# Kernel optimization log

Measured on AMD Instinct MI355X. Metric: run time of the kernel, lower is better.

The kernel has to match this reference:

```python
import jax, jax.numpy as jnp
from jax import lax
import numpy as np

BLOCK = 256
EPS = 1e-6


def rms_norm(x, w):
    var = jnp.mean(jnp.square(x), axis=-1, keepdims=True)
    return x * lax.rsqrt(var + EPS) * w


def lightning_attn(q, k, v, slope):
    # q,k,v: [b,h,n,d]; slope: [h] positive decay rates
    b, h, n, d = q.shape
    nb = n // BLOCK
    ar = jnp.arange(1, BLOCK + 1, dtype=q.dtype)          # [BLOCK]
    s = slope[:, None, None]                               # [h,1,1]
    q_decay = jnp.exp(-s * ar[:, None])                    # [h,BLOCK,1]
    k_decay = jnp.exp(-s * (BLOCK - ar)[:, None])          # [h,BLOCK,1]
    idx = ar[:, None] - ar[None, :]                        # [BLOCK,BLOCK]
    diag_decay = jnp.exp(jnp.where(idx >= 0, -s * idx, -jnp.inf))  # [h,B,B]
    block_decay = jnp.exp(-slope * BLOCK)[None, :, None, None]     # [1,h,1,1]

    def to_blocks(x):
        return jnp.moveaxis(x.reshape(b, h, nb, BLOCK, d), 2, 0)   # [nb,b,h,B,d]

    qb, kb, vb = to_blocks(q), to_blocks(k), to_blocks(v)

    def step(kv, blk):
        qi, ki, vi = blk                                   # [b,h,B,d]
        inter = jnp.einsum('bhmd,bhde->bhme', qi * q_decay, kv)
        qk = jnp.einsum('bhmd,bhkd->bhmk', qi, ki) * diag_decay
        intra = jnp.einsum('bhmk,bhke->bhme', qk, vi)
        kv_new = block_decay * kv + jnp.einsum('bhmd,bhme->bhde', ki * k_decay, vi)
        return kv_new, inter + intra

    kv0 = jnp.zeros((b, h, d, d), q.dtype)
    kv, out = lax.scan(step, kv0, (qb, kb, vb))            # out: [nb,b,h,B,d]
    out = jnp.moveaxis(out, 0, 2).reshape(b, h, n, d)
    return out, kv


def setup_inputs() -> dict:
    key = jax.random.key(0)
    ks = jax.random.split(key, 6)
    b, n, hidden, h, dh = 2, 4096, 2048, 16, 128
    return {
        'hidden_states': jax.random.normal(ks[0], (b, n, hidden), jnp.float32),
        'slope_rate': jax.random.uniform(ks[1], (h,), jnp.float32, 1e-3, 0.2),
        'w_qkv': jax.random.normal(ks[2], (3 * h * dh, hidden), jnp.float32) * 0.02,
        'w_gate': jax.random.normal(ks[3], (h * dh, hidden), jnp.float32) * 0.02,
        'w_out': jax.random.normal(ks[4], (hidden, h * dh), jnp.float32) * 0.02,
        'norm_w': jnp.ones((h * dh,), jnp.float32),
    }


def reference(hidden_states, slope_rate, w_qkv, w_gate, w_out, norm_w):
    b, n, hidden = hidden_states.shape
    h = slope_rate.shape[0]
    dh = hidden // h
    qkv = jax.nn.silu(hidden_states @ w_qkv.T)             # [b,n,3*h*dh]
    qkv = qkv.reshape(b, n, 3, h, dh)
    q = jnp.transpose(qkv[:, :, 0], (0, 2, 1, 3))          # [b,h,n,dh]
    k = jnp.transpose(qkv[:, :, 1], (0, 2, 1, 3))
    v = jnp.transpose(qkv[:, :, 2], (0, 2, 1, 3))
    attn_out, _kv = lightning_attn(q, k, v, slope_rate)
    attn_out = jnp.transpose(attn_out, (0, 2, 1, 3)).reshape(b, n, h * dh)
    out = rms_norm(attn_out, norm_w)
    gate = jax.nn.sigmoid(hidden_states @ w_gate.T)
    out = (gate * out) @ w_out.T
    return out
```

## Files before the change

kernel.cpp:

```cpp
#include <hip/hip_runtime.h>


typedef unsigned short u16;
typedef __bf16 bf16x8 __attribute__((ext_vector_type(8)));
typedef float f32x4 __attribute__((ext_vector_type(4)));

#define SEQ 4096
#define HID 2048

__device__ __forceinline__ u16 f2bf(float f) {
    union { float f; unsigned u; } v; v.f = f;
    unsigned r = v.u + 0x7fffu + ((v.u >> 16) & 1u);
    return (u16)(r >> 16);
}
__device__ __forceinline__ float bf2f(u16 u) {
    union { unsigned u; float f; } v; v.u = ((unsigned)u) << 16; return v.f;
}

typedef __attribute__((address_space(1))) unsigned char gas_u8;
typedef __attribute__((address_space(3))) unsigned char las_u8;
__device__ __forceinline__ void gld16(const void* g, void* l) {
    __builtin_amdgcn_global_load_lds((gas_u8*)g, (las_u8*)l, 16, 0, 0);
}

__global__ __launch_bounds__(256) void castk3(const float* __restrict__ a, u16* __restrict__ ao,
                                              const float* __restrict__ b, u16* __restrict__ bo,
                                              const float* __restrict__ c, u16* __restrict__ co) {
    const int bid = blockIdx.x;
    const float* src; u16* dst; size_t i;
    if (bid < 16384)      { src = a; dst = ao; i = (size_t)bid * 256 + threadIdx.x; }
    else if (bid < 28672) { src = b; dst = bo; i = (size_t)(bid - 16384) * 256 + threadIdx.x; }
    else                  { src = c; dst = co; i = (size_t)(bid - 28672) * 256 + threadIdx.x; }
    const float4 f = *(const float4*)&src[i * 4];
    uint2 o;
    o.x = (unsigned)f2bf(f.x) | ((unsigned)f2bf(f.y) << 16);
    o.y = (unsigned)f2bf(f.z) | ((unsigned)f2bf(f.w) << 16);
    *(uint2*)&dst[i * 4] = o;
}

template <int MODE>
__global__ __launch_bounds__(512, 2) void gemm256(const u16* __restrict__ A,
                                                  const u16* __restrict__ Bm,
                                                  void* __restrict__ Cv,
                                                  void* __restrict__ aux,
                                                  void* __restrict__ aux2) {
    constexpr int NTN = (MODE == 0) ? 32 : 8;
    constexpr int NT  = 32;
    extern __shared__ u16 smem[];

    const int bid = blockIdx.x;
    const int xcd = bid & 7, l = bid >> 3;
    int tm, tn;
    if constexpr (MODE == 0) {
        tm = xcd * 4 + (l & 3);
        tn = ((l >> 2) & 7) | ((l >> 5) << 3);
    } else {
        const int wgid = xcd * 32 + l;
        tm = wgid / NTN; tn = wgid % NTN;
    }

    const int tid  = threadIdx.x;
    const int lane = tid & 63, wv = tid >> 6;
    const int quad = lane >> 4, cl = lane & 15;
    const int wm = (wv & 1) * 128, wn = (wv >> 1) * 64;

    const int srw  = tid >> 3;
    const int colo = ((tid & 7) ^ (srw & 7)) * 8;
    const u16* gA0 = A  + (size_t)(tm * 256 + srw) * HID + colo;
    const u16* gB0 = Bm + (size_t)(tn * 256 + srw) * HID + colo;

    const int x0 = ((quad       ^ (cl & 7)) * 8);
    const int x1 = (((4 + quad) ^ (cl & 7)) * 8);

    f32x4 acc[8][4];
    const f32x4 zero = {0.f, 0.f, 0.f, 0.f};
    #pragma unroll
    for (int a = 0; a < 8; a++)
        #pragma unroll
        for (int b = 0; b < 4; b++) acc[a][b] = zero;

    bf16x8 af[8], b0[4], b1[4];

    auto STG = [&](int kt, int mat, int hh) {
        const u16* g = (mat ? gB0 : gA0) + (size_t)(hh * 128) * HID + kt * 64;
        u16* lp = smem + (kt & 1) * 32768 + mat * 16384 + hh * 8192 + wv * 512;
        gld16(g, lp);
        gld16(g + (size_t)64 * HID, lp + 4096);
    };
    auto LDA = [&](int qm, int ab) {
        #pragma unroll
        for (int mi = 0; mi < 4; mi++) {
            const int rr = (wm + qm * 64 + mi * 16 + cl) * 64 + ab;
            af[mi * 2 + 0] = *(const bf16x8*)&smem[rr + x0];
            af[mi * 2 + 1] = *(const bf16x8*)&smem[rr + x1];
        }
    };
    auto LDB = [&](bf16x8* d, int qn, int bb2) {
        #pragma unroll
        for (int ni = 0; ni < 2; ni++) {
            const int rr = (wn + qn * 32 + ni * 16 + cl) * 64 + bb2;
            d[ni * 2 + 0] = *(const bf16x8*)&smem[rr + x0];
            d[ni * 2 + 1] = *(const bf16x8*)&smem[rr + x1];
        }
    };
    auto MM = [&](int qm, int qn, const bf16x8* bv) {
        #pragma unroll
        for (int mi = 0; mi < 4; mi++)
            #pragma unroll
            for (int ni = 0; ni < 2; ni++) {
                f32x4 c = acc[qm * 4 + mi][qn * 2 + ni];
                c = __builtin_amdgcn_mfma_f32_16x16x32_bf16(af[mi * 2 + 0], bv[ni * 2 + 0], c, 0, 0, 0);
                c = __builtin_amdgcn_mfma_f32_16x16x32_bf16(af[mi * 2 + 1], bv[ni * 2 + 1], c, 0, 0, 0);
                acc[qm * 4 + mi][qn * 2 + ni] = c;
            }
    };

    STG(0, 1, 0); STG(0, 1, 1); STG(0, 0, 0); STG(0, 0, 1);
    STG(1, 1, 0); STG(1, 1, 1); STG(1, 0, 0);
    asm volatile("s_waitcnt vmcnt(6)" ::: "memory");
    __builtin_amdgcn_s_barrier();
    LDA(0, 0); LDB(b0, 0, 16384);

    #pragma unroll 2
    for (int t = 0; t < NT; ++t) {
        const int ab  = (t & 1) * 32768;
        const int bb2 = ab + 16384;
        const int nab = ((t + 1) & 1) * 32768;
        if (t + 1 < NT) STG(t + 1, 0, 1);
        __builtin_amdgcn_s_barrier();
        asm volatile("s_waitcnt lgkmcnt(0)" ::: "memory");
        __builtin_amdgcn_s_setprio(1); MM(0, 0, b0); __builtin_amdgcn_s_setprio(0);
        LDB(b1, 1, bb2);
        __builtin_amdgcn_s_barrier();
        if (t + 2 < NT) STG(t + 2, 1, 0);
        __builtin_amdgcn_s_barrier();
        asm volatile("s_waitcnt lgkmcnt(0)" ::: "memory");
        __builtin_amdgcn_s_setprio(1); MM(0, 1, b1); __builtin_amdgcn_s_setprio(0);
        LDA(1, ab);
        __builtin_amdgcn_s_barrier();
        if (t + 2 < NT) STG(t + 2, 1, 1);
        __builtin_amdgcn_s_barrier();
        asm volatile("s_waitcnt lgkmcnt(0)" ::: "memory");
        __builtin_amdgcn_s_setprio(1); MM(1, 1, b1); __builtin_amdgcn_s_setprio(0);
        __builtin_amdgcn_s_barrier();
        if (t + 2 < NT) {
            STG(t + 2, 0, 0);
            asm volatile("s_waitcnt vmcnt(6)" ::: "memory");
        } else {
            asm volatile("s_waitcnt vmcnt(0)" ::: "memory");
        }
        __builtin_amdgcn_s_barrier();
        __builtin_amdgcn_s_setprio(1); MM(1, 0, b0); __builtin_amdgcn_s_setprio(0);
        if (t + 1 < NT) { LDA(0, nab); LDB(b0, 0, nab + 16384); }
        __builtin_amdgcn_s_barrier();
    }

    if constexpr (MODE == 0) {
        const int grp = tn * 2 + (wn >> 7);
        const int which = grp >> 4, hd = grp & 15;
        const int n64 = wn & 64;
        if (which == 2) {
            const size_t bz = (size_t)((tm >> 4) * 256 + hd * 16 + (tm & 15));
            u16* tdst = (u16*)aux + bz * 32768;
            #pragma unroll
            for (int a = 0; a < 8; a++) {
                const int mm = wm + (a >> 2) * 64 + (a & 3) * 16 + quad * 4;
                #pragma unroll
                for (int b = 0; b < 4; b++) {
                    const int d = n64 + (b >> 1) * 32 + (b & 1) * 16 + cl;
                    u16 p[4];
                    #pragma unroll
                    for (int r = 0; r < 4; r++) {
                        const float x = acc[a][b][r];
                        p[r] = f2bf(x / (1.f + __expf(-x)));
                    }
                    uint2 pk;
                    pk.x = (unsigned)p[0] | ((unsigned)p[1] << 16);
                    pk.y = (unsigned)p[2] | ((unsigned)p[3] << 16);
                    *(uint2*)&tdst[(size_t)d * 256 + mm] = pk;
                }
            }
            return;
        }
        u16* dst = (which == 0) ? (u16*)Cv
                 : (which == 1) ? (u16*)Cv + (size_t)16777216
                                : (u16*)aux2;
        #pragma unroll
        for (int a = 0; a < 8; a++)
            #pragma unroll
            for (int b = 0; b < 4; b++)
                #pragma unroll
                for (int r = 0; r < 4; r++) {
                    const int m = tm * 256 + wm + (a >> 2) * 64 + (a & 3) * 16 + quad * 4 + r;
                    const int col = hd * 128 + n64 + (b >> 1) * 32 + (b & 1) * 16 + cl;
                    const float x = acc[a][b][r];
                    const float v = (which == 3) ? 1.f / (1.f + __expf(-x))
                                                 : x / (1.f + __expf(-x));
                    dst[(size_t)m * HID + col] = f2bf(v);
                }
        return;
    } else {
        float* C = (float*)Cv;
        #pragma unroll
        for (int a = 0; a < 8; a++)
            #pragma unroll
            for (int b = 0; b < 4; b++)
                #pragma unroll
                for (int r = 0; r < 4; r++) {
                    const int m = tm * 256 + wm + (a >> 2) * 64 + (a & 3) * 16 + quad * 4 + r;
                    const int n = tn * 256 + wn + (b >> 1) * 32 + (b & 1) * 16 + cl;
                    C[(size_t)m * HID + n] = acc[a][b][r];
                }
    }
}

#define M_KVT   4

template <int MODE>
__global__ __launch_bounds__(256) void gemm_nt(const u16* __restrict__ A,
                                               const u16* __restrict__ Bm,
                                               void* __restrict__ Cv,
                                               const float* __restrict__ slope,
                                               int bz0,
                                               void* __restrict__ aux,
                                               void* __restrict__ aux2) {
    const int tid = threadIdx.x;
    const int bz  = blockIdx.z + bz0;

    __shared__ u16 smem[16384];

    const int lane = tid & 63, wv = tid >> 6;
    const int wm = (wv & 1) * 64, wn = (wv >> 1) * 64;
    const int quad = lane >> 4, cl = lane & 15;
    const int lr = lane >> 2;
    const int lc = (lane & 3) * 8;

    f32x4 acc[4][4];
    const f32x4 zero = {0.f, 0.f, 0.f, 0.f};
    #pragma unroll
    for (int mi = 0; mi < 4; mi++)
        #pragma unroll
        for (int ni = 0; ni < 4; ni++) acc[mi][ni] = zero;

    const u16* gA = A  + (size_t)bz * 32768 + (size_t)(wv * 32 + lr) * 256 + lc;
    const u16* gB = Bm + (size_t)bz * 32768 + (size_t)(wv * 32 + lr) * 256 + lc;

    auto stage = [&](int c, int buf) {
        u16* lA = smem + buf * 8192 + wv * 1024;
        u16* lB = lA + 4096;
        const int k0 = c * 32;
        gld16(gA + k0,                    lA);
        gld16(gA + k0 + (size_t)16 * 256, lA + 512);
        gld16(gB + k0,                    lB);
        gld16(gB + k0 + (size_t)16 * 256, lB + 512);
    };

    stage(0, 0);
    for (int c = 0; c < 8; ++c) {
        const int cb = c & 1;
        if (c + 1 < 8) {
            stage(c + 1, cb ^ 1);
            asm volatile("s_waitcnt vmcnt(4)" ::: "memory");
        } else {
            asm volatile("s_waitcnt vmcnt(0)" ::: "memory");
        }
        __builtin_amdgcn_s_barrier();
        const u16* As = smem + cb * 8192;
        const u16* Bs = As + 4096;
        const int ko = quad * 8;
        bf16x8 af[4], bfv[4];
        #pragma unroll
        for (int mi = 0; mi < 4; mi++) af[mi] = *(const bf16x8*)&As[(wm + mi * 16 + cl) * 32 + ko];
        #pragma unroll
        for (int ni = 0; ni < 4; ni++) bfv[ni] = *(const bf16x8*)&Bs[(wn + ni * 16 + cl) * 32 + ko];
        #pragma unroll
        for (int mi = 0; mi < 4; mi++)
            #pragma unroll
            for (int ni = 0; ni < 4; ni++)
                acc[mi][ni] = __builtin_amdgcn_mfma_f32_16x16x32_bf16(af[mi], bfv[ni], acc[mi][ni], 0, 0, 0);
        __builtin_amdgcn_s_barrier();
    }

    #pragma unroll
    for (int mi = 0; mi < 4; mi++)
        #pragma unroll
        for (int ni = 0; ni < 4; ni++)
            #pragma unroll
            for (int r = 0; r < 4; r++) {
                const int m = wm + mi * 16 + quad * 4 + r;
                const int n = wn + ni * 16 + cl;
                ((float*)Cv)[(size_t)bz * 16384 + m * 128 + n] = acc[mi][ni][r];
            }
}

__global__ __launch_bounds__(256) void fused_pv(const u16* __restrict__ qb,
                                                const u16* __restrict__ kb,
                                                const u16* __restrict__ ST,
                                                const u16* __restrict__ vT,
                                                u16* __restrict__ attn,
                                                const float* __restrict__ slope) {
    __shared__ u16 smem[36864];
    u16* q_lds = smem;
    u16* k_lds = smem + 16384;
    u16* P_lds = smem + 24576;
    u16* Bs    = smem + 28672;

    const int tm = blockIdx.x;
    const int bz = blockIdx.z;
    const int bb = bz >> 8, hh = (bz >> 4) & 15, jb = bz & 15;
    const float s_ = slope[hh];

    const int tid  = threadIdx.x;
    const int lane = tid & 63, wv = tid >> 6;
    const int quad = lane >> 4, cl = lane & 15;
    const int wm = (wv & 1) * 64, wn = (wv >> 1) * 64;
    const int lr = lane >> 2, lc = (lane & 3) * 8;
    const int pcb = (wv >> 1) * 16;

    const size_t rowbase = (size_t)(bb * SEQ + jb * 256);

    const u16* gq = qb + (rowbase + tm * 128 + wv * 32 + lr) * HID + hh * 128 + lc;
    u16* lq = q_lds + wv * 1024 + lr * 32 + lc;
    #pragma unroll
    for (int ks = 0; ks < 4; ks++) {
        gld16(gq + ks * 32,                 lq + ks * 4096);
        gld16(gq + ks * 32 + 16 * HID,      lq + ks * 4096 + 512);
    }

    f32x4 acc[4][4];
    const f32x4 zero = {0.f, 0.f, 0.f, 0.f};
    #pragma unroll
    for (int mi = 0; mi < 4; mi++)
        #pragma unroll
        for (int ni = 0; ni < 4; ni++) acc[mi][ni] = zero;

    const u16* gS = ST + (size_t)bz * 16384 + (size_t)(wv * 32 + lr) * 128 + lc;
    auto stage_st = [&](int ks, int buf) {
        u16* lB = Bs + buf * 4096 + wv * 1024 + lr * 32 + lc;
        gld16(gS + ks * 32,            lB);
        gld16(gS + ks * 32 + 16 * 128, lB + 512);
    };
    stage_st(0, 0);
    #pragma unroll
    for (int ks = 0; ks < 4; ks++) {
        const int sb = ks & 1;
        if (ks + 1 < 4) {
            stage_st(ks + 1, sb ^ 1);
            asm volatile("s_waitcnt vmcnt(2)" ::: "memory");
        } else {
            asm volatile("s_waitcnt vmcnt(0)" ::: "memory");
        }
        __builtin_amdgcn_s_barrier();
        bf16x8 af[4], bfv[4];
        #pragma unroll
        for (int mi = 0; mi < 4; mi++)
            af[mi] = *(const bf16x8*)&q_lds[ks * 4096 + (wm + mi * 16 + cl) * 32 + quad * 8];
        #pragma unroll
        for (int ni = 0; ni < 4; ni++)
            bfv[ni] = *(const bf16x8*)&Bs[sb * 4096 + (wn + ni * 16 + cl) * 32 + quad * 8];
        #pragma unroll
        for (int mi = 0; mi < 4; mi++)
            #pragma unroll
            for (int ni = 0; ni < 4; ni++)
                acc[mi][ni] = __builtin_amdgcn_mfma_f32_16x16x32_bf16(af[mi], bfv[ni], acc[mi][ni], 0, 0, 0);
        __builtin_amdgcn_s_barrier();
    }
    #pragma unroll
    for (int mi = 0; mi < 4; mi++)
        #pragma unroll
        for (int r = 0; r < 4; r++) {
            const int m = tm * 128 + wm + mi * 16 + quad * 4 + r;
            const float qd = __expf(-s_ * (float)(m + 1));
            #pragma unroll
            for (int ni = 0; ni < 4; ni++) acc[mi][ni][r] *= qd;
        }

    const int kmax = (tm == 0) ? 128 : 256;
    const int nc   = kmax >> 5;
    const u16* gV = vT + (size_t)bz * 32768 + (size_t)(wv * 32 + lr) * 256 + lc;
    const int krow = tid >> 4;
    const int kcol = (((tid & 15) ^ (krow & 7)) * 8);
    const int kvr = pcb + cl;

    auto stage_chunk = [&](int c, int buf) {
        u16* lk = k_lds + buf * 4096 + wv * 512 + lane * 8;
        u16* lv = Bs + buf * 4096 + wv * 1024 + lr * 32 + lc;
        const int kv0 = c * 32;
        gld16(kb + (rowbase + kv0 +      krow) * HID + hh * 128 + kcol, lk);
        gld16(kb + (rowbase + kv0 + 16 + krow) * HID + hh * 128 + kcol, lk + 2048);
        gld16(gV + kv0,            lv);
        gld16(gV + kv0 + 16 * 256, lv + 512);
    };

    stage_chunk(0, 0);
    for (int c = 0; c < nc; ++c) {
        const int cb = c & 1;
        if (c + 1 < nc) {
            stage_chunk(c + 1, cb ^ 1);
            asm volatile("s_waitcnt vmcnt(4)" ::: "memory");
        } else {
            asm volatile("s_waitcnt vmcnt(0)" ::: "memory");
        }
        __builtin_amdgcn_s_barrier();
        f32x4 acc2[4];
        #pragma unroll
        for (int mi = 0; mi < 4; mi++) acc2[mi] = zero;
        #pragma unroll
        for (int ds = 0; ds < 4; ds++) {
            bf16x8 bk = *(const bf16x8*)&k_lds[cb * 4096 + kvr * 128 + (((ds * 4 + quad) ^ (kvr & 7)) * 8)];
            #pragma unroll
            for (int mi = 0; mi < 4; mi++) {
                bf16x8 aq = *(const bf16x8*)&q_lds[ds * 4096 + (wm + mi * 16 + cl) * 32 + quad * 8];
                acc2[mi] = __builtin_amdgcn_mfma_f32_16x16x32_bf16(aq, bk, acc2[mi], 0, 0, 0);
            }
        }
        const int kv0 = c * 32;
        #pragma unroll
        for (int mi = 0; mi < 4; mi++)
            #pragma unroll
            for (int r = 0; r < 4; r++) {
                const int row = wm + mi * 16 + quad * 4 + r;
                const int mb  = tm * 128 + row;
                const int kv  = kv0 + pcb + cl;
                const int d   = mb - kv;
                const float x = acc2[mi][r];
                P_lds[row * 32 + pcb + cl] = f2bf(d >= 0 ? x * __expf(-s_ * (float)d) : 0.f);
            }
        asm volatile("s_waitcnt lgkmcnt(0)" ::: "memory");
        __builtin_amdgcn_s_barrier();
        bf16x8 afp[4], bfv[4];
        #pragma unroll
        for (int mi = 0; mi < 4; mi++)
            afp[mi] = *(const bf16x8*)&P_lds[(wm + mi * 16 + cl) * 32 + quad * 8];
        #pragma unroll
        for (int ni = 0; ni < 4; ni++)
            bfv[ni] = *(const bf16x8*)&Bs[cb * 4096 + (wn + ni * 16 + cl) * 32 + quad * 8];
        #pragma unroll
        for (int mi = 0; mi < 4; mi++)
            #pragma unroll
            for (int ni = 0; ni < 4; ni++)
                acc[mi][ni] = __builtin_amdgcn_mfma_f32_16x16x32_bf16(afp[mi], bfv[ni], acc[mi][ni], 0, 0, 0);
        __builtin_amdgcn_s_barrier();
    }

    #pragma unroll
    for (int mi = 0; mi < 4; mi++)
        #pragma unroll
        for (int ni = 0; ni < 4; ni++)
            #pragma unroll
            for (int r = 0; r < 4; r++) {
                const int m = tm * 128 + wm + mi * 16 + quad * 4 + r;
                const int n = wn + ni * 16 + cl;
                attn[(rowbase + m) * HID + hh * 128 + n] = f2bf(acc[mi][ni][r]);
            }
}

__global__ __launch_bounds__(256) void transpose_k(const u16* __restrict__ kb,
                                                   u16* __restrict__ kTs,
                                                   const float* __restrict__ slope) {
    __shared__ u16 t[128][137];
    const int bz = blockIdx.x;
    const int bb = bz >> 8, hh = (bz >> 4) & 15, jb = bz & 15;
    const int tid = threadIdx.x;
    const float s_ = slope[hh];
    const u16* src = kb + ((size_t)(bb * SEQ + jb * 256)) * HID + hh * 128;
    u16* dst = kTs + (size_t)bz * 32768;

    for (int half = 0; half < 2; half++) {
        #pragma unroll
        for (int i = 0; i < 8; i++) {
            const int flat = tid + 256 * i;
            const int row = flat >> 4, c8 = (flat & 15) * 8;
            *(uint4*)&t[row][c8] = *(const uint4*)&src[(size_t)(half * 128 + row) * HID + c8];
        }
        __syncthreads();
        #pragma unroll
        for (int i = 0; i < 8; i++) {
            const int flat = tid + 256 * i;
            const int d = flat >> 4, mc = (flat & 15) * 8;
            u16 p[8];
            #pragma unroll
            for (int j = 0; j < 8; j++) {
                const int m = half * 128 + mc + j;
                p[j] = f2bf(bf2f(t[mc + j][d]) * __expf(-s_ * (float)(255 - m)));
            }
            uint4 pk;
            pk.x = (unsigned)p[0] | ((unsigned)p[1] << 16);
            pk.y = (unsigned)p[2] | ((unsigned)p[3] << 16);
            pk.z = (unsigned)p[4] | ((unsigned)p[5] << 16);
            pk.w = (unsigned)p[6] | ((unsigned)p[7] << 16);
            *(uint4*)&dst[(size_t)d * 256 + half * 128 + mc] = pk;
        }
        __syncthreads();
    }
}

__global__ __launch_bounds__(256) void scan_kv(const float* __restrict__ KVT,
                                               u16* __restrict__ ST,
                                               const float* __restrict__ slope) {
    const int bh = blockIdx.x >> 4, ch = blockIdx.x & 15;
    const int off = ch * 1024 + threadIdx.x * 4;
    const float bd = __expf(-256.f * slope[bh & 15]);
    float4 st = {0.f, 0.f, 0.f, 0.f};
    for (int j = 0; j < 16; j++) {
        const size_t base = ((size_t)(bh * 16 + j)) * 16384 + off;
        uint2 o;
        o.x = (unsigned)f2bf(st.x) | ((unsigned)f2bf(st.y) << 16);
        o.y = (unsigned)f2bf(st.z) | ((unsigned)f2bf(st.w) << 16);
        *(uint2*)&ST[base] = o;
        const float4 kv = *(const float4*)&KVT[base];
        st.x = bd * st.x + kv.x;
        st.y = bd * st.y + kv.y;
        st.z = bd * st.z + kv.z;
        st.w = bd * st.w + kv.w;
    }
}

__global__ __launch_bounds__(256) void rmsnorm_gate(const u16* __restrict__ attn,
                                                    const u16* __restrict__ gate,
                                                    const float* __restrict__ nw,
                                                    u16* __restrict__ y,
                                                    const float* __restrict__ wout,
                                                    u16* __restrict__ wout_bf) {
    const int r = blockIdx.x, tid = threadIdx.x;

    {
        const size_t wi = (size_t)r * 512 + tid * 2;
        const float2 wf = *(const float2*)&wout[wi];
        *(unsigned*)&wout_bf[wi] = (unsigned)f2bf(wf.x) | ((unsigned)f2bf(wf.y) << 16);
    }

    const size_t base = (size_t)r * HID + tid * 8;
    const uint4 a = *(const uint4*)&attn[base];
    float x[8];
    x[0] = bf2f(a.x & 0xffff); x[1] = bf2f(a.x >> 16);
    x[2] = bf2f(a.y & 0xffff); x[3] = bf2f(a.y >> 16);
    x[4] = bf2f(a.z & 0xffff); x[5] = bf2f(a.z >> 16);
    x[6] = bf2f(a.w & 0xffff); x[7] = bf2f(a.w >> 16);
    float s = 0.f;
    #pragma unroll
    for (int i = 0; i < 8; i++) s += x[i] * x[i];
    #pragma unroll
    for (int off = 32; off > 0; off >>= 1) s += __shfl_down(s, off);
    __shared__ float red[4];
    if ((tid & 63) == 0) red[tid >> 6] = s;
    __syncthreads();
    const float tot = red[0] + red[1] + red[2] + red[3];
    const float sc = rsqrtf(tot * (1.f / 2048.f) + 1e-6f);
    const uint4 g = *(const uint4*)&gate[base];
    float gv[8];
    gv[0] = bf2f(g.x & 0xffff); gv[1] = bf2f(g.x >> 16);
    gv[2] = bf2f(g.y & 0xffff); gv[3] = bf2f(g.y >> 16);
    gv[4] = bf2f(g.z & 0xffff); gv[5] = bf2f(g.z >> 16);
    gv[6] = bf2f(g.w & 0xffff); gv[7] = bf2f(g.w >> 16);
    const float4 w0 = *(const float4*)&nw[tid * 8];
    const float4 w1 = *(const float4*)&nw[tid * 8 + 4];
    const float wv[8] = {w0.x, w0.y, w0.z, w0.w, w1.x, w1.y, w1.z, w1.w};
    u16 o[8];
    #pragma unroll
    for (int i = 0; i < 8; i++) o[i] = f2bf(gv[i] * x[i] * sc * wv[i]);
    uint4 ov;
    ov.x = (unsigned)o[0] | ((unsigned)o[1] << 16);
    ov.y = (unsigned)o[2] | ((unsigned)o[3] << 16);
    ov.z = (unsigned)o[4] | ((unsigned)o[5] << 16);
    ov.w = (unsigned)o[6] | ((unsigned)o[7] << 16);
    *(uint4*)&y[base] = ov;
}

extern "C" void kernel_launch(void* const* d_in, const int* in_sizes, int n_in,
                              void* d_out, int out_size, void* d_ws, size_t ws_size,
                              hipStream_t stream) {
    const float* hidden = (const float*)d_in[0];
    const float* slope  = (const float*)d_in[1];
    const float* w_qkv  = (const float*)d_in[2];
    const float* w_gate = (const float*)d_in[3];
    const float* w_out  = (const float*)d_in[4];
    const float* norm_w = (const float*)d_in[5];
    float* out = (float*)d_out;

    char* w = (char*)d_ws;
    u16* qb   = (u16*)(w);
    u16* kb   = (u16*)(w +  33554432);
    u16* kTs  = (u16*)(w +  67108864);
    u16* hid_bf = (u16*)(w + 100663296);
    u16* vT   = (u16*)(w + 134217728);
    u16* gate = (u16*)(w + 167772160);
    u16* wqkv_bf  = (u16*)(w + 201326592);
    u16* wgate_bf = (u16*)(w + 201326592 + 25165824);
    float* KVT  = (float*)hid_bf;
    u16*   ST   = kTs;
    u16*   wout_bf = kb;
    u16*   attn = wqkv_bf;
    u16*   y    = kTs;

    static bool s_attr = false;
    if (!s_attr) {
        (void)hipFuncSetAttribute((const void*)gemm256<0>,
                                  hipFuncAttributeMaxDynamicSharedMemorySize, 131072);
        (void)hipFuncSetAttribute((const void*)gemm256<1>,
                                  hipFuncAttributeMaxDynamicSharedMemorySize, 131072);
        s_attr = true;
    }

    castk3<<<32768, 256, 0, stream>>>(hidden, hid_bf, w_qkv, wqkv_bf, w_gate, wgate_bf);

    gemm256<0><<<dim3(1024), dim3(512), 131072, stream>>>(hid_bf, wqkv_bf, qb, vT, gate);
    transpose_k     <<<512,             256, 0, stream>>>(kb, kTs, slope);
    gemm_nt<M_KVT ><<<dim3(1, 1, 512),  256, 0, stream>>>(vT, kTs, KVT, slope, 0, nullptr, nullptr);
    scan_kv         <<<512,             256, 0, stream>>>(KVT, ST, slope);
    fused_pv        <<<dim3(2, 1, 512), 256, 0, stream>>>(qb, kb, ST, vT, attn, slope);
    rmsnorm_gate    <<<8192,            256, 0, stream>>>(attn, gate, norm_w, y, w_out, wout_bf);
    gemm256<1><<<dim3(256), dim3(512), 131072, stream>>>(y, wout_bf, (void*)out, nullptr, nullptr);
}
```

Before: 441.6 us.

## Fuse K transpose and decay scaling into the per-block KV GEMM

Removes the separate transpose_k kernel, which wrote a decayed, transposed copy of K to global memory. The KV-state GEMM now loads K tiles directly from the row-major qkv buffer into XOR-swizzled LDS. Each lane gathers its transposed fragment from LDS and applies the exponential k-decay before the MFMA. This saves one launch plus a full global write and read of K, at the cost of scalar LDS gathers and extra ALU work inside the GEMM loop.

```diff
diff --git a/kernel.cpp b/kernel.cpp
--- a/kernel.cpp
+++ b/kernel.cpp
@@ -214,26 +214,25 @@
     }
 }
 
-#define M_KVT   4
-
-template <int MODE>
-__global__ __launch_bounds__(256) void gemm_nt(const u16* __restrict__ A,
-                                               const u16* __restrict__ Bm,
-                                               void* __restrict__ Cv,
-                                               const float* __restrict__ slope,
-                                               int bz0,
-                                               void* __restrict__ aux,
-                                               void* __restrict__ aux2) {
+__global__ __launch_bounds__(256) void kvt_fused(const u16* __restrict__ vT,
+                                                 const u16* __restrict__ kb,
+                                                 float* __restrict__ KVT,
+                                                 const float* __restrict__ slope) {
+    __shared__ u16 smem[16384];
+
     const int tid = threadIdx.x;
-    const int bz  = blockIdx.z + bz0;
-
-    __shared__ u16 smem[16384];
+    const int bz  = blockIdx.x;
+    const int bb = bz >> 8, hh = (bz >> 4) & 15, jb = bz & 15;
+    const float s_ = slope[hh];
+    const float es = __expf(s_);
+    const size_t rowbase = (size_t)(bb * SEQ + jb * 256);
 
     const int lane = tid & 63, wv = tid >> 6;
     const int wm = (wv & 1) * 64, wn = (wv >> 1) * 64;
     const int quad = lane >> 4, cl = lane & 15;
     const int lr = lane >> 2;
     const int lc = (lane & 3) * 8;
+    const int ko = quad * 8;
 
     f32x4 acc[4][4];
     const f32x4 zero = {0.f, 0.f, 0.f, 0.f};
@@ -242,17 +241,17 @@
         #pragma unroll
         for (int ni = 0; ni < 4; ni++) acc[mi][ni] = zero;
 
-    const u16* gA = A  + (size_t)bz * 32768 + (size_t)(wv * 32 + lr) * 256 + lc;
-    const u16* gB = Bm + (size_t)bz * 32768 + (size_t)(wv * 32 + lr) * 256 + lc;
+    const u16* gA = vT + (size_t)bz * 32768 + (size_t)(wv * 32 + lr) * 256 + lc;
+    const u16* gK = kb + (rowbase + (tid >> 4)) * HID + hh * 128
+                       + (((tid & 15) ^ (tid >> 4)) * 8);
 
     auto stage = [&](int c, int buf) {
-        u16* lA = smem + buf * 8192 + wv * 1024;
-        u16* lB = lA + 4096;
-        const int k0 = c * 32;
-        gld16(gA + k0,                    lA);
-        gld16(gA + k0 + (size_t)16 * 256, lA + 512);
-        gld16(gB + k0,                    lB);
-        gld16(gB + k0 + (size_t)16 * 256, lB + 512);
+        u16* lA = smem + buf * 4096 + wv * 1024;
+        gld16(gA + c * 32,                    lA);
+        gld16(gA + c * 32 + (size_t)16 * 256, lA + 512);
+        u16* lB = smem + 8192 + buf * 4096 + wv * 512 + lane * 8;
+        gld16(gK + (size_t)(c * 32) * HID,      lB);
+        gld16(gK + (size_t)(c * 32 + 16) * HID, lB + 2048);
     };
 
     stage(0, 0);
@@ -265,14 +264,29 @@
             asm volatile("s_waitcnt vmcnt(0)" ::: "memory");
         }
         __builtin_amdgcn_s_barrier();
-        const u16* As = smem + cb * 8192;
-        const u16* Bs = As + 4096;
-        const int ko = quad * 8;
+        const u16* As   = smem + cb * 4096;
+        const u16* braw = smem + 8192 + cb * 4096;
+        const int kv0 = c * 32;
+        const float dec0 = __expf(-s_ * (float)(255 - (kv0 + ko)));
         bf16x8 af[4], bfv[4];
         #pragma unroll
-        for (int mi = 0; mi < 4; mi++) af[mi] = *(const bf16x8*)&As[(wm + mi * 16 + cl) * 32 + ko];
-        #pragma unroll
-        for (int ni = 0; ni < 4; ni++) bfv[ni] = *(const bf16x8*)&Bs[(wn + ni * 16 + cl) * 32 + ko];
+        for (int mi = 0; mi < 4; mi++)
+            af[mi] = *(const bf16x8*)&As[(wm + mi * 16 + cl) * 32 + ko];
+        #pragma unroll
+        for (int ni = 0; ni < 4; ni++) {
+            const int d   = wn + ni * 16 + cl;
+            const int dhi = d >> 3, dlo = d & 7;
+            float dec = dec0;
+            union { u16 u[8]; bf16x8 v; } cvt;
+            #pragma unroll
+            for (int j = 0; j < 8; j++) {
+                const int ml = ko + j;
+                const u16 raw = braw[ml * 128 + ((dhi ^ (ml & 15)) * 8) + dlo];
+                cvt.u[j] = f2bf(bf2f(raw) * dec);
+                dec *= es;
+            }
+            bfv[ni] = cvt.v;
+        }
         #pragma unroll
         for (int mi = 0; mi < 4; mi++)
             #pragma unroll
@@ -289,7 +303,7 @@
             for (int r = 0; r < 4; r++) {
                 const int m = wm + mi * 16 + quad * 4 + r;
                 const int n = wn + ni * 16 + cl;
-                ((float*)Cv)[(size_t)bz * 16384 + m * 128 + n] = acc[mi][ni][r];
+                KVT[(size_t)bz * 16384 + m * 128 + n] = acc[mi][ni][r];
             }
 }
 
@@ -453,46 +467,6 @@
                 const int n = wn + ni * 16 + cl;
                 attn[(rowbase + m) * HID + hh * 128 + n] = f2bf(acc[mi][ni][r]);
             }
-}
-
-__global__ __launch_bounds__(256) void transpose_k(const u16* __restrict__ kb,
-                                                   u16* __restrict__ kTs,
-                                                   const float* __restrict__ slope) {
-    __shared__ u16 t[128][137];
-    const int bz = blockIdx.x;
-    const int bb = bz >> 8, hh = (bz >> 4) & 15, jb = bz & 15;
-    const int tid = threadIdx.x;
-    const float s_ = slope[hh];
-    const u16* src = kb + ((size_t)(bb * SEQ + jb * 256)) * HID + hh * 128;
-    u16* dst = kTs + (size_t)bz * 32768;
-
-    for (int half = 0; half < 2; half++) {
-        #pragma unroll
-        for (int i = 0; i < 8; i++) {
-            const int flat = tid + 256 * i;
-            const int row = flat >> 4, c8 = (flat & 15) * 8;
-            *(uint4*)&t[row][c8] = *(const uint4*)&src[(size_t)(half * 128 + row) * HID + c8];
-        }
-        __syncthreads();
-        #pragma unroll
-        for (int i = 0; i < 8; i++) {
-            const int flat = tid + 256 * i;
-            const int d = flat >> 4, mc = (flat & 15) * 8;
-            u16 p[8];
-            #pragma unroll
-            for (int j = 0; j < 8; j++) {
-                const int m = half * 128 + mc + j;
-                p[j] = f2bf(bf2f(t[mc + j][d]) * __expf(-s_ * (float)(255 - m)));
-            }
-            uint4 pk;
-            pk.x = (unsigned)p[0] | ((unsigned)p[1] << 16);
-            pk.y = (unsigned)p[2] | ((unsigned)p[3] << 16);
-            pk.z = (unsigned)p[4] | ((unsigned)p[5] << 16);
-            pk.w = (unsigned)p[6] | ((unsigned)p[7] << 16);
-            *(uint4*)&dst[(size_t)d * 256 + half * 128 + mc] = pk;
-        }
-        __syncthreads();
-    }
 }
 
 __global__ __launch_bounds__(256) void scan_kv(const float* __restrict__ KVT,
@@ -605,8 +579,7 @@
     castk3<<<32768, 256, 0, stream>>>(hidden, hid_bf, w_qkv, wqkv_bf, w_gate, wgate_bf);
 
     gemm256<0><<<dim3(1024), dim3(512), 131072, stream>>>(hid_bf, wqkv_bf, qb, vT, gate);
-    transpose_k     <<<512,             256, 0, stream>>>(kb, kTs, slope);
-    gemm_nt<M_KVT ><<<dim3(1, 1, 512),  256, 0, stream>>>(vT, kTs, KVT, slope, 0, nullptr, nullptr);
+    kvt_fused       <<<512,             256, 0, stream>>>(vT, kb, KVT, slope);
     scan_kv         <<<512,             256, 0, stream>>>(KVT, ST, slope);
     fused_pv        <<<dim3(2, 1, 512), 256, 0, stream>>>(qb, kb, ST, vT, attn, slope);
     rmsnorm_gate    <<<8192,            256, 0, stream>>>(attn, gate, norm_w, y, w_out, wout_bf);
```

Result: faster. 430.6 us (-2.5%).
